# Kernel tuning notes

Hardware: AMD Instinct MI355X
Metric: run time of the kernel (lower is better)

## Reference

```python
import jax, jax.numpy as jnp
import numpy as np
import math

# ---- static configuration (matches init_kwargs) ----
METADATA = [64, 48, 32]   # channels per l = 0,1,2
MAX_L = 3                 # order_out
N_BATCH = 32768
fact = math.factorial

def _cg_complex(l1, m1, l2, m2, l3, m3):
    # Clebsch-Gordan coefficient <l1 m1 l2 m2 | l3 m3> via Racah formula
    if m1 + m2 != m3 or l3 < abs(l1 - l2) or l3 > l1 + l2:
        return 0.0
    pre = math.sqrt((2*l3+1) * fact(l1+l2-l3) * fact(l1-l2+l3) * fact(-l1+l2+l3) / fact(l1+l2+l3+1))
    pre *= math.sqrt(fact(l1+m1)*fact(l1-m1)*fact(l2+m2)*fact(l2-m2)*fact(l3+m3)*fact(l3-m3))
    kmin = max(0, l2-l3-m1, l1-l3+m2)
    kmax = min(l1+l2-l3, l1-m1, l2+m2)
    s = 0.0
    for k in range(kmin, kmax+1):
        s += (-1)**k / (fact(k)*fact(l1+l2-l3-k)*fact(l1-m1-k)*fact(l2+m2-k)*fact(l3-l2+m1+k)*fact(l3-l1-m2+k))
    return pre * s

def _U(l):
    # complex->real spherical harmonic change of basis, rows = real m', cols = complex m
    U = np.zeros((2*l+1, 2*l+1), dtype=np.complex128)
    for m in range(-l, l+1):
        r = m + l
        if m > 0:
            U[r, m+l] = (-1)**m / math.sqrt(2.0); U[r, -m+l] = 1.0/math.sqrt(2.0)
        elif m == 0:
            U[r, l] = 1.0
        else:
            U[r, m+l] = 1j/math.sqrt(2.0); U[r, -m+l] = -1j*(-1)**m/math.sqrt(2.0)
    return U

def _real_cg(l1, l2, l3):
    Cc = np.zeros((2*l1+1, 2*l2+1, 2*l3+1))
    for m1 in range(-l1, l1+1):
        for m2 in range(-l2, l2+1):
            for m3 in range(-l3, l3+1):
                Cc[m1+l1, m2+l2, m3+l3] = _cg_complex(l1, m1, l2, m2, l3, m3)
    T = np.einsum('am,bn,co,mno->abc', _U(l1), _U(l2), _U(l3).conj(), Cc.astype(np.complex128))
    T = T.imag if np.abs(T.imag).max() > np.abs(T.real).max() else T.real
    return np.ascontiguousarray(T).astype(np.float32)

# ---- static index structures ----
L_IN = len(METADATA)
OFF_IN = np.concatenate([[0], np.cumsum([METADATA[l]*(2*l+1) for l in range(L_IN)])]).astype(np.int64)
DIM_IN = int(OFF_IN[-1])  # 368
PATHS = []
for l1 in range(L_IN):
    for l2 in range(L_IN):
        for l3 in range(abs(l1-l2), min(l1+l2, MAX_L)+1):
            PATHS.append((l1, l2, l3, min(METADATA[l1], METADATA[l2])))
MD_OV = [0]*(MAX_L+1)
for (_, _, l3, ch) in PATHS:
    MD_OV[l3] = max(MD_OV[l3], ch)
OFF_OUT = np.concatenate([[0], np.cumsum([MD_OV[l]*(2*l+1) for l in range(MAX_L+1)])]).astype(np.int64)
DIM_OUT = int(OFF_OUT[-1])  # 672
CG = {(l1, l2, l3): jnp.asarray(_real_cg(l1, l2, l3)) for (l1, l2, l3, _) in PATHS}

_mix_id, _scat = [], []
_base = 0
for (l1, l2, l3, ch) in PATHS:
    for i in range(ch):
        for m in range(2*l3+1):
            _mix_id.append(_base + i)
            _scat.append(int(OFF_OUT[l3]) + i*(2*l3+1) + m)
    _base += ch
MIX_ID = jnp.asarray(np.array(_mix_id, dtype=np.int64))
SCATTER = jnp.asarray(np.array(_scat, dtype=np.int64))
N_MIX = _base  # 688

_chan_in = []
_cb = 0
for l in range(L_IN):
    for i in range(METADATA[l]):
        _chan_in += [_cb + i]*(2*l+1)
    _cb += METADATA[l]
CHAN_IN = jnp.asarray(np.array(_chan_in, dtype=np.int64))
N_KEEP = _cb  # 144
_kin, _kout = [], []
for l in range(L_IN):
    cp = min(METADATA[l], MD_OV[l])
    for i in range(cp):
        for m in range(2*l+1):
            _kin.append(int(OFF_IN[l]) + i*(2*l+1) + m)
            _kout.append(int(OFF_OUT[l]) + i*(2*l+1) + m)
KEEP_IN = jnp.asarray(np.array(_kin, dtype=np.int64))
KEEP_OUT = jnp.asarray(np.array(_kout, dtype=np.int64))

SQ3 = math.sqrt(3.0)

def setup_inputs() -> dict:
    key = jax.random.key(0)
    k1, k2, k3 = jax.random.split(key, 3)
    x = jax.random.normal(k1, (N_BATCH, DIM_IN), dtype=jnp.float32)
    keep_coeff = jax.random.uniform(k2, (N_KEEP,), minval=-SQ3, maxval=SQ3, dtype=jnp.float32)
    mix_coeff = jax.random.uniform(k3, (N_MIX,), minval=-SQ3, maxval=SQ3, dtype=jnp.float32)
    return {"x": x, "keep_coeff": keep_coeff, "mix_coeff": mix_coeff}

def reference(x, keep_coeff, mix_coeff):
    n = x.shape[0]
    # keep path: per-channel coeff broadcast over m components
    x_keep = x * keep_coeff[CHAN_IN]  # [N, 368]
    # CG tensor-product self-coupling (diagonal channel pairing per path)
    tps = []
    for (l1, l2, l3, ch) in PATHS:
        x1 = x[:, OFF_IN[l1]:OFF_IN[l1]+ch*(2*l1+1)].reshape(n, ch, 2*l1+1)
        x2 = x[:, OFF_IN[l2]:OFF_IN[l2]+ch*(2*l2+1)].reshape(n, ch, 2*l2+1)
        tps.append(jnp.einsum('nia,nib,abm->nim', x1, x2, CG[(l1, l2, l3)]).reshape(n, -1))
    cat = jnp.concatenate(tps, axis=1)  # [N, 2576] non-overlapped TP output
    cat = cat * 0.5 * mix_coeff[MIX_ID]
    # scatter (index_add) into overlapped output layout
    out = jnp.zeros((n, DIM_OUT), dtype=x.dtype).at[:, SCATTER].add(cat)
    # gather + add of keep path (index_select + add_)
    out = out.at[:, KEEP_OUT].add(x_keep[:, KEEP_IN])
    return out
```

## Files before the change

### kernel.cpp

```cpp
#include <hip/hip_runtime.h>


namespace cgc {

struct cplx { double re, im; };
constexpr cplx cmul(cplx a, cplx b){ return {a.re*b.re - a.im*b.im, a.re*b.im + a.im*b.re}; }

constexpr double cfact(int n){ double r = 1.0; for (int i = 2; i <= n; ++i) r *= i; return r; }
constexpr double cabsd(double x){ return x < 0 ? -x : x; }

constexpr double csqrtd(double x){
  if (x <= 0.0) return 0.0;
  double g = x > 1.0 ? x : 1.0;
  for (int i = 0; i < 48; ++i) g = 0.5*(g + x/g);
  return g;
}

constexpr double SQRT2 = csqrtd(2.0);

constexpr double cg_complex(int l1,int m1,int l2,int m2,int l3,int m3){
  if (m1 + m2 != m3) return 0.0;
  int lo = l1 > l2 ? l1 - l2 : l2 - l1;
  if (l3 < lo || l3 > l1 + l2) return 0.0;
  double pre = csqrtd((2*l3+1) * cfact(l1+l2-l3)*cfact(l1-l2+l3)*cfact(-l1+l2+l3)/cfact(l1+l2+l3+1));
  pre *= csqrtd(cfact(l1+m1)*cfact(l1-m1)*cfact(l2+m2)*cfact(l2-m2)*cfact(l3+m3)*cfact(l3-m3));
  int kmin = 0;
  if (l2-l3-m1 > kmin) kmin = l2-l3-m1;
  if (l1-l3+m2 > kmin) kmin = l1-l3+m2;
  int kmax = l1+l2-l3;
  if (l1-m1 < kmax) kmax = l1-m1;
  if (l2+m2 < kmax) kmax = l2+m2;
  double s = 0.0;
  for (int k = kmin; k <= kmax; ++k){
    double d = cfact(k)*cfact(l1+l2-l3-k)*cfact(l1-m1-k)*cfact(l2+m2-k)
             * cfact(l3-l2+m1+k)*cfact(l3-l1-m2+k);
    s += ((k & 1) ? -1.0 : 1.0) / d;
  }
  return pre * s;
}

constexpr cplx Uent(int l, int r, int c){
  int m = r - l;
  if (m > 0){
    if (c ==  m + l) return { ((m & 1) ? -1.0 : 1.0)/SQRT2, 0.0 };
    if (c == -m + l) return { 1.0/SQRT2, 0.0 };
    return {0.0, 0.0};
  } else if (m == 0){
    if (c == l) return {1.0, 0.0};
    return {0.0, 0.0};
  } else {
    int ma = -m;
    if (c ==  m + l) return { 0.0, 1.0/SQRT2 };
    if (c == -m + l) return { 0.0, -(((ma & 1) ? -1.0 : 1.0))/SQRT2 };
    return {0.0, 0.0};
  }
}

template<int L1,int L2,int L3>
struct CGData { float w[(2*L1+1)*(2*L2+1)*(2*L3+1)]; };

template<int L1,int L2,int L3>
constexpr CGData<L1,L2,L3> make_cg(){
  constexpr int D1 = 2*L1+1, D2 = 2*L2+1, D3 = 2*L3+1;
  cplx U1[D1*D1] = {}; cplx U2[D2*D2] = {}; cplx U3c[D3*D3] = {};
  for (int r = 0; r < D1; ++r) for (int c = 0; c < D1; ++c) U1[r*D1+c] = Uent(L1, r, c);
  for (int r = 0; r < D2; ++r) for (int c = 0; c < D2; ++c) U2[r*D2+c] = Uent(L2, r, c);
  for (int r = 0; r < D3; ++r) for (int c = 0; c < D3; ++c){
    cplx u = Uent(L3, r, c); u.im = -u.im; U3c[r*D3+c] = u;
  }
  double Cc[D1*D2*D3] = {};
  for (int m1 = -L1; m1 <= L1; ++m1)
    for (int m2 = -L2; m2 <= L2; ++m2){
      int m3 = m1 + m2;
      if (m3 < -L3 || m3 > L3) continue;
      Cc[((m1+L1)*D2 + (m2+L2))*D3 + (m3+L3)] = cg_complex(L1,m1,L2,m2,L3,m3);
    }
  double re[D1*D2*D3] = {}; double im[D1*D2*D3] = {};
  for (int a = 0; a < D1; ++a)
    for (int b = 0; b < D2; ++b)
      for (int c = 0; c < D3; ++c){
        double sre = 0.0, sim = 0.0;
        for (int m = 0; m < D1; ++m)
          for (int n = 0; n < D2; ++n){
            int o = m + n - L1 - L2 + L3;
            if (o < 0 || o >= D3) continue;
            double cc = Cc[(m*D2+n)*D3 + o];
            if (cc == 0.0) continue;
            cplx p = cmul(cmul(U1[a*D1+m], U2[b*D2+n]), U3c[c*D3+o]);
            sre += p.re * cc; sim += p.im * cc;
          }
        re[(a*D2+b)*D3+c] = sre; im[(a*D2+b)*D3+c] = sim;
      }
  double mre = 0.0, mim = 0.0;
  for (int k = 0; k < D1*D2*D3; ++k){
    if (cabsd(re[k]) > mre) mre = cabsd(re[k]);
    if (cabsd(im[k]) > mim) mim = cabsd(im[k]);
  }
  CGData<L1,L2,L3> outv{};
  for (int k = 0; k < D1*D2*D3; ++k){
    double v = (mim > mre) ? im[k] : re[k];
    outv.w[k] = (cabsd(v) < 1e-10) ? 0.0f : (float)v;
  }
  return outv;
}

}

template<int L1,int L2,int L3>
__device__ __forceinline__ void tp_path(const float* xa, const float* xb, float cmix, float* acc){
  constexpr cgc::CGData<L1,L2,L3> cg = cgc::make_cg<L1,L2,L3>();
  constexpr int D1 = 2*L1+1, D2 = 2*L2+1, D3 = 2*L3+1;
  #pragma unroll
  for (int a = 0; a < D1; ++a){
    #pragma unroll
    for (int b = 0; b < D2; ++b){
      const float pr = xa[a] * xb[b];
      #pragma unroll
      for (int m = 0; m < D3; ++m){
        const float W = cg.w[(a*D2+b)*D3 + m];
        if (W != 0.0f) acc[m] += (cmix * W) * pr;
      }
    }
  }
}


__global__ __launch_bounds__(256) void selfmix_kernel(
    const float* __restrict__ x, const float* __restrict__ keep,
    const float* __restrict__ mix, float* __restrict__ out, int n)
{
  const long long gid = (long long)blockIdx.x * 256 + threadIdx.x;
  const long long nA = (long long)n * 32;
  const long long nB = (long long)n * 16;

  if (gid < nA){
    const int i   = (int)(gid & 31);
    const int row = (int)(gid >> 5);
    const float* xr = x + (long long)row * 368;
    float*     orow = out + (long long)row * 672;
    float s = xr[i];
    float p[3], d[5];
    #pragma unroll
    for (int k = 0; k < 3; ++k) p[k] = xr[64 + i*3 + k];
    #pragma unroll
    for (int k = 0; k < 5; ++k) d[k] = xr[208 + i*5 + k];

    float o0 = 0.f;
    float o1[3] = {0.f,0.f,0.f};
    float o2[5] = {0.f,0.f,0.f,0.f,0.f};
    float o3[7] = {0.f,0.f,0.f,0.f,0.f,0.f,0.f};

    tp_path<0,0,0>(&s,&s, 0.5f*mix[  0+i], &o0);
    tp_path<0,1,1>(&s, p, 0.5f*mix[ 64+i],  o1);
    tp_path<0,2,2>(&s, d, 0.5f*mix[112+i],  o2);
    tp_path<1,0,1>( p,&s, 0.5f*mix[144+i],  o1);
    tp_path<1,1,0>( p, p, 0.5f*mix[192+i], &o0);
    tp_path<1,1,1>( p, p, 0.5f*mix[240+i],  o1);
    tp_path<1,1,2>( p, p, 0.5f*mix[288+i],  o2);
    tp_path<1,2,1>( p, d, 0.5f*mix[336+i],  o1);
    tp_path<1,2,2>( p, d, 0.5f*mix[368+i],  o2);
    tp_path<1,2,3>( p, d, 0.5f*mix[400+i],  o3);
    tp_path<2,0,2>( d,&s, 0.5f*mix[432+i],  o2);
    tp_path<2,1,1>( d, p, 0.5f*mix[464+i],  o1);
    tp_path<2,1,2>( d, p, 0.5f*mix[496+i],  o2);
    tp_path<2,1,3>( d, p, 0.5f*mix[528+i],  o3);
    tp_path<2,2,0>( d, d, 0.5f*mix[560+i], &o0);
    tp_path<2,2,1>( d, d, 0.5f*mix[592+i],  o1);
    tp_path<2,2,2>( d, d, 0.5f*mix[624+i],  o2);
    tp_path<2,2,3>( d, d, 0.5f*mix[656+i],  o3);

    o0 += keep[i] * s;
    const float k1 = keep[64+i], k2 = keep[112+i];
    #pragma unroll
    for (int k = 0; k < 3; ++k) o1[k] += k1 * p[k];
    #pragma unroll
    for (int k = 0; k < 5; ++k) o2[k] += k2 * d[k];

    orow[i] = o0;
    #pragma unroll
    for (int k = 0; k < 3; ++k) orow[ 64 + i*3 + k] = o1[k];
    #pragma unroll
    for (int k = 0; k < 5; ++k) orow[208 + i*5 + k] = o2[k];
    #pragma unroll
    for (int k = 0; k < 7; ++k) orow[448 + i*7 + k] = o3[k];

  } else if (gid < nA + nB){
    const long long t = gid - nA;
    const int i   = 32 + (int)(t & 15);
    const int row = (int)(t >> 4);
    const float* xr = x + (long long)row * 368;
    float*     orow = out + (long long)row * 672;
    float s = xr[i];
    float p[3];
    #pragma unroll
    for (int k = 0; k < 3; ++k) p[k] = xr[64 + i*3 + k];

    float o0 = 0.f;
    float o1[3] = {0.f,0.f,0.f};
    float o2[5] = {0.f,0.f,0.f,0.f,0.f};

    tp_path<0,0,0>(&s,&s, 0.5f*mix[  0+i], &o0);
    tp_path<0,1,1>(&s, p, 0.5f*mix[ 64+i],  o1);
    tp_path<1,0,1>( p,&s, 0.5f*mix[144+i],  o1);
    tp_path<1,1,0>( p, p, 0.5f*mix[192+i], &o0);
    tp_path<1,1,1>( p, p, 0.5f*mix[240+i],  o1);
    tp_path<1,1,2>( p, p, 0.5f*mix[288+i],  o2);

    o0 += keep[i] * s;
    const float k1 = keep[64+i];
    #pragma unroll
    for (int k = 0; k < 3; ++k) o1[k] += k1 * p[k];

    orow[i] = o0;
    #pragma unroll
    for (int k = 0; k < 3; ++k) orow[ 64 + i*3 + k] = o1[k];
    #pragma unroll
    for (int k = 0; k < 5; ++k) orow[208 + i*5 + k] = o2[k];

  } else if (gid < nA + 2*nB){
    const long long t = gid - nA - nB;
    const int i   = 48 + (int)(t & 15);
    const int row = (int)(t >> 4);
    const float* xr = x + (long long)row * 368;
    float s = xr[i];
    float o0 = 0.f;
    tp_path<0,0,0>(&s,&s, 0.5f*mix[0+i], &o0);
    o0 += keep[i] * s;
    out[(long long)row * 672 + i] = o0;
  }
}

extern "C" void kernel_launch(void* const* d_in, const int* in_sizes, int n_in,
                              void* d_out, int out_size, void* d_ws, size_t ws_size,
                              hipStream_t stream)
{
  const float* x    = (const float*)d_in[0];
  const float* keep = (const float*)d_in[1];
  const float* mix  = (const float*)d_in[2];
  float* out = (float*)d_out;
  const int n = in_sizes[0] / 368;
  const long long total = (long long)n * 64;
  const int blocks = (int)((total + 255) / 256);
  selfmix_kernel<<<blocks, 256, 0, stream>>>(x, keep, mix, out, n);
}
```

Before: 135.5 us.

## Stage rows through shared memory with coalesced float4 loads and stores

Each block now processes four whole rows: it copies the input rows into LDS with float4 loads, computes the tensor-product paths reading from and writing to LDS, then writes the full output rows back with coalesced float4 stores. This targets the uncoalesced strided global accesses of the per-thread layout. It adds two block barriers and 16 KB of LDS per block, which may limit occupancy.

```diff
diff --git a/kernel.cpp b/kernel.cpp
--- a/kernel.cpp
+++ b/kernel.cpp
@@ -125,108 +125,136 @@
 }
 
 
+#define ROWS_PER_BLOCK 4
+
 __global__ __launch_bounds__(256) void selfmix_kernel(
     const float* __restrict__ x, const float* __restrict__ keep,
     const float* __restrict__ mix, float* __restrict__ out, int n)
 {
-  const long long gid = (long long)blockIdx.x * 256 + threadIdx.x;
-  const long long nA = (long long)n * 32;
-  const long long nB = (long long)n * 16;
-
-  if (gid < nA){
-    const int i   = (int)(gid & 31);
-    const int row = (int)(gid >> 5);
-    const float* xr = x + (long long)row * 368;
-    float*     orow = out + (long long)row * 672;
-    float s = xr[i];
-    float p[3], d[5];
-    #pragma unroll
-    for (int k = 0; k < 3; ++k) p[k] = xr[64 + i*3 + k];
-    #pragma unroll
-    for (int k = 0; k < 5; ++k) d[k] = xr[208 + i*5 + k];
-
-    float o0 = 0.f;
-    float o1[3] = {0.f,0.f,0.f};
-    float o2[5] = {0.f,0.f,0.f,0.f,0.f};
-    float o3[7] = {0.f,0.f,0.f,0.f,0.f,0.f,0.f};
-
-    tp_path<0,0,0>(&s,&s, 0.5f*mix[  0+i], &o0);
-    tp_path<0,1,1>(&s, p, 0.5f*mix[ 64+i],  o1);
-    tp_path<0,2,2>(&s, d, 0.5f*mix[112+i],  o2);
-    tp_path<1,0,1>( p,&s, 0.5f*mix[144+i],  o1);
-    tp_path<1,1,0>( p, p, 0.5f*mix[192+i], &o0);
-    tp_path<1,1,1>( p, p, 0.5f*mix[240+i],  o1);
-    tp_path<1,1,2>( p, p, 0.5f*mix[288+i],  o2);
-    tp_path<1,2,1>( p, d, 0.5f*mix[336+i],  o1);
-    tp_path<1,2,2>( p, d, 0.5f*mix[368+i],  o2);
-    tp_path<1,2,3>( p, d, 0.5f*mix[400+i],  o3);
-    tp_path<2,0,2>( d,&s, 0.5f*mix[432+i],  o2);
-    tp_path<2,1,1>( d, p, 0.5f*mix[464+i],  o1);
-    tp_path<2,1,2>( d, p, 0.5f*mix[496+i],  o2);
-    tp_path<2,1,3>( d, p, 0.5f*mix[528+i],  o3);
-    tp_path<2,2,0>( d, d, 0.5f*mix[560+i], &o0);
-    tp_path<2,2,1>( d, d, 0.5f*mix[592+i],  o1);
-    tp_path<2,2,2>( d, d, 0.5f*mix[624+i],  o2);
-    tp_path<2,2,3>( d, d, 0.5f*mix[656+i],  o3);
-
-    o0 += keep[i] * s;
-    const float k1 = keep[64+i], k2 = keep[112+i];
-    #pragma unroll
-    for (int k = 0; k < 3; ++k) o1[k] += k1 * p[k];
-    #pragma unroll
-    for (int k = 0; k < 5; ++k) o2[k] += k2 * d[k];
-
-    orow[i] = o0;
-    #pragma unroll
-    for (int k = 0; k < 3; ++k) orow[ 64 + i*3 + k] = o1[k];
-    #pragma unroll
-    for (int k = 0; k < 5; ++k) orow[208 + i*5 + k] = o2[k];
-    #pragma unroll
-    for (int k = 0; k < 7; ++k) orow[448 + i*7 + k] = o3[k];
-
-  } else if (gid < nA + nB){
-    const long long t = gid - nA;
-    const int i   = 32 + (int)(t & 15);
-    const int row = (int)(t >> 4);
-    const float* xr = x + (long long)row * 368;
-    float*     orow = out + (long long)row * 672;
-    float s = xr[i];
-    float p[3];
-    #pragma unroll
-    for (int k = 0; k < 3; ++k) p[k] = xr[64 + i*3 + k];
-
-    float o0 = 0.f;
-    float o1[3] = {0.f,0.f,0.f};
-    float o2[5] = {0.f,0.f,0.f,0.f,0.f};
-
-    tp_path<0,0,0>(&s,&s, 0.5f*mix[  0+i], &o0);
-    tp_path<0,1,1>(&s, p, 0.5f*mix[ 64+i],  o1);
-    tp_path<1,0,1>( p,&s, 0.5f*mix[144+i],  o1);
-    tp_path<1,1,0>( p, p, 0.5f*mix[192+i], &o0);
-    tp_path<1,1,1>( p, p, 0.5f*mix[240+i],  o1);
-    tp_path<1,1,2>( p, p, 0.5f*mix[288+i],  o2);
-
-    o0 += keep[i] * s;
-    const float k1 = keep[64+i];
-    #pragma unroll
-    for (int k = 0; k < 3; ++k) o1[k] += k1 * p[k];
-
-    orow[i] = o0;
-    #pragma unroll
-    for (int k = 0; k < 3; ++k) orow[ 64 + i*3 + k] = o1[k];
-    #pragma unroll
-    for (int k = 0; k < 5; ++k) orow[208 + i*5 + k] = o2[k];
-
-  } else if (gid < nA + 2*nB){
-    const long long t = gid - nA - nB;
-    const int i   = 48 + (int)(t & 15);
-    const int row = (int)(t >> 4);
-    const float* xr = x + (long long)row * 368;
-    float s = xr[i];
-    float o0 = 0.f;
-    tp_path<0,0,0>(&s,&s, 0.5f*mix[0+i], &o0);
-    o0 += keep[i] * s;
-    out[(long long)row * 672 + i] = o0;
+  __shared__ __align__(16) float xs[ROWS_PER_BLOCK * 368];
+  __shared__ __align__(16) float os[ROWS_PER_BLOCK * 672];
+
+  const int t = threadIdx.x;
+  const long long blk  = blockIdx.x;
+  const long long row0 = blk * ROWS_PER_BLOCK;
+
+  {
+    const long long nf4_in   = (long long)n * 92;
+    const long long base_in  = blk * (ROWS_PER_BLOCK * 92);
+    const float4* __restrict__ src = (const float4*)x;
+    float4* dst = (float4*)xs;
+    if (base_in + t < nf4_in)               dst[t]       = src[base_in + t];
+    if (t < 112 && base_in + 256 + t < nf4_in) dst[256+t] = src[base_in + 256 + t];
+  }
+  __syncthreads();
+
+  if (t < 128){
+    const int rowL = t >> 5;
+    const int i    = t & 31;
+    if (row0 + rowL < n){
+      const float* xr = xs + rowL*368;
+      float*     orow = os + rowL*672;
+      float s = xr[i];
+      float p[3], d[5];
+      #pragma unroll
+      for (int k = 0; k < 3; ++k) p[k] = xr[64 + i*3 + k];
+      #pragma unroll
+      for (int k = 0; k < 5; ++k) d[k] = xr[208 + i*5 + k];
+
+      float o0 = 0.f;
+      float o1[3] = {0.f,0.f,0.f};
+      float o2[5] = {0.f,0.f,0.f,0.f,0.f};
+      float o3[7] = {0.f,0.f,0.f,0.f,0.f,0.f,0.f};
+
+      tp_path<0,0,0>(&s,&s, 0.5f*mix[  0+i], &o0);
+      tp_path<0,1,1>(&s, p, 0.5f*mix[ 64+i],  o1);
+      tp_path<0,2,2>(&s, d, 0.5f*mix[112+i],  o2);
+      tp_path<1,0,1>( p,&s, 0.5f*mix[144+i],  o1);
+      tp_path<1,1,0>( p, p, 0.5f*mix[192+i], &o0);
+      tp_path<1,1,1>( p, p, 0.5f*mix[240+i],  o1);
+      tp_path<1,1,2>( p, p, 0.5f*mix[288+i],  o2);
+      tp_path<1,2,1>( p, d, 0.5f*mix[336+i],  o1);
+      tp_path<1,2,2>( p, d, 0.5f*mix[368+i],  o2);
+      tp_path<1,2,3>( p, d, 0.5f*mix[400+i],  o3);
+      tp_path<2,0,2>( d,&s, 0.5f*mix[432+i],  o2);
+      tp_path<2,1,1>( d, p, 0.5f*mix[464+i],  o1);
+      tp_path<2,1,2>( d, p, 0.5f*mix[496+i],  o2);
+      tp_path<2,1,3>( d, p, 0.5f*mix[528+i],  o3);
+      tp_path<2,2,0>( d, d, 0.5f*mix[560+i], &o0);
+      tp_path<2,2,1>( d, d, 0.5f*mix[592+i],  o1);
+      tp_path<2,2,2>( d, d, 0.5f*mix[624+i],  o2);
+      tp_path<2,2,3>( d, d, 0.5f*mix[656+i],  o3);
+
+      o0 += keep[i] * s;
+      const float k1 = keep[64+i], k2 = keep[112+i];
+      #pragma unroll
+      for (int k = 0; k < 3; ++k) o1[k] += k1 * p[k];
+      #pragma unroll
+      for (int k = 0; k < 5; ++k) o2[k] += k2 * d[k];
+
+      orow[i] = o0;
+      #pragma unroll
+      for (int k = 0; k < 3; ++k) orow[ 64 + i*3 + k] = o1[k];
+      #pragma unroll
+      for (int k = 0; k < 5; ++k) orow[208 + i*5 + k] = o2[k];
+      #pragma unroll
+      for (int k = 0; k < 7; ++k) orow[448 + i*7 + k] = o3[k];
+    }
+  } else if (t < 192){
+    const int rowL = (t - 128) >> 4;
+    const int i    = 32 + (t & 15);
+    if (row0 + rowL < n){
+      const float* xr = xs + rowL*368;
+      float*     orow = os + rowL*672;
+      float s = xr[i];
+      float p[3];
+      #pragma unroll
+      for (int k = 0; k < 3; ++k) p[k] = xr[64 + i*3 + k];
+
+      float o0 = 0.f;
+      float o1[3] = {0.f,0.f,0.f};
+      float o2[5] = {0.f,0.f,0.f,0.f,0.f};
+
+      tp_path<0,0,0>(&s,&s, 0.5f*mix[  0+i], &o0);
+      tp_path<0,1,1>(&s, p, 0.5f*mix[ 64+i],  o1);
+      tp_path<1,0,1>( p,&s, 0.5f*mix[144+i],  o1);
+      tp_path<1,1,0>( p, p, 0.5f*mix[192+i], &o0);
+      tp_path<1,1,1>( p, p, 0.5f*mix[240+i],  o1);
+      tp_path<1,1,2>( p, p, 0.5f*mix[288+i],  o2);
+
+      o0 += keep[i] * s;
+      const float k1 = keep[64+i];
+      #pragma unroll
+      for (int k = 0; k < 3; ++k) o1[k] += k1 * p[k];
+
+      orow[i] = o0;
+      #pragma unroll
+      for (int k = 0; k < 3; ++k) orow[ 64 + i*3 + k] = o1[k];
+      #pragma unroll
+      for (int k = 0; k < 5; ++k) orow[208 + i*5 + k] = o2[k];
+    }
+  } else {
+    const int rowL = (t - 192) >> 4;
+    const int i    = 48 + (t & 15);
+    if (row0 + rowL < n){
+      const float* xr = xs + rowL*368;
+      float s = xr[i];
+      float o0 = 0.f;
+      tp_path<0,0,0>(&s,&s, 0.5f*mix[0+i], &o0);
+      o0 += keep[i] * s;
+      os[rowL*672 + i] = o0;
+    }
+  }
+  __syncthreads();
+
+  {
+    const long long nf4_out  = (long long)n * 168;
+    const long long base_out = blk * (ROWS_PER_BLOCK * 168);
+    const float4* srco = (const float4*)os;
+    float4* __restrict__ dsto = (float4*)out;
+    if (base_out + t < nf4_out)                 dsto[base_out + t]       = srco[t];
+    if (base_out + 256 + t < nf4_out)           dsto[base_out + 256 + t] = srco[256+t];
+    if (t < 160 && base_out + 512 + t < nf4_out) dsto[base_out + 512 + t] = srco[512+t];
   }
 }
 
@@ -239,7 +267,6 @@
   const float* mix  = (const float*)d_in[2];
   float* out = (float*)d_out;
   const int n = in_sizes[0] / 368;
-  const long long total = (long long)n * 64;
-  const int blocks = (int)((total + 255) / 256);
+  const int blocks = (n + ROWS_PER_BLOCK - 1) / ROWS_PER_BLOCK;
   selfmix_kernel<<<blocks, 256, 0, stream>>>(x, keep, mix, out, n);
 }
```

Result: slower. 147.3 us (+8.7%).
